# Kernel tuning notes

Hardware: AMD Instinct MI355X
Metric: run time of the kernel (lower is better)

Reference implementation:

```python
import jax, jax.numpy as jnp
import numpy as np

# Quantization constants (mirror the torch module's __init__ kwargs)
INPUT_SCALE = 0.0625          # q_in: Quantize(input_scale, 0, qint8)
SCORE_SCALE = 0.00390625      # npu_matmul output_scale for scores (1/256)
PROB_SCALE = 0.00048828125    # q_probs: Quantize(prob_scale, 0, qint8) (1/2048)
I8_MIN, I8_MAX = -128, 127
I16_MIN, I16_MAX = -32768, 32767

D, K, M, N = 256, 256, 256, 65536  # w1:[K,D], x:[D,N], w2:[M,K]


def quantize_i8(x, scale):
    # torch Quantize: round-half-to-even(x/scale) + zp(=0), clamp to int8
    return jnp.clip(jnp.round(x / scale), I8_MIN, I8_MAX).astype(jnp.int8)


def npu_matmul_i16(w_i8, x_i8):
    acc = jnp.matmul(w_i8.astype(jnp.int32), x_i8.astype(jnp.int32))
    return jnp.clip(acc, I16_MIN, I16_MAX).astype(jnp.int16)


def setup_inputs() -> dict:
    key = jax.random.key(0)
    k1, k2, k3 = jax.random.split(key, 3)
    x = jax.random.normal(k1, (D, N), dtype=jnp.float32)
    # weights are pre-quantized int8 values stored as float32 (as in the torch module)
    w1 = jax.random.randint(k2, (K, D), -16, 16).astype(jnp.float32)
    w2 = jax.random.randint(k3, (M, K), -16, 16).astype(jnp.float32)
    return {"x": x, "w1": w1, "w2": w2}


def reference(x, w1, w2):
    x_q = quantize_i8(x, INPUT_SCALE)                       # [D, N] int8
    scores_q = npu_matmul_i16(w1.astype(jnp.int8), x_q)     # [K, N] int16 (quantized, scale=SCORE_SCALE)
    scores = scores_q.astype(jnp.float32) * SCORE_SCALE     # dequantize
    probs = jax.nn.softmax(scores, axis=0)                  # softmax over dim 0
    q_probs = quantize_i8(probs, PROB_SCALE)                # [K, N] int8
    out = npu_matmul_i16(w2.astype(jnp.int8), q_probs)      # [M, N] int16
    return out
```

## Files before the change

### kernel.cpp

```cpp
#include <hip/hip_runtime.h>

typedef int   int4v   __attribute__((ext_vector_type(4)));
typedef float float4v __attribute__((ext_vector_type(4)));

#define N_DIM 65536

__device__ __forceinline__ int quant8(float v) {
    int q = (int)rintf(v);
    q = q > 127 ? 127 : q;
    q = q < -128 ? -128 : q;
    return q;
}

__device__ __forceinline__ int clamp16(int s) {
    s = s > 32767 ? 32767 : s;
    s = s < -32768 ? -32768 : s;
    return s;
}

__device__ __forceinline__ unsigned int qpack(float4v v) {
    int q0 = quant8(v.x * 16.0f);
    int q1 = quant8(v.y * 16.0f);
    int q2 = quant8(v.z * 16.0f);
    int q3 = quant8(v.w * 16.0f);
    return (unsigned int)((q0 & 0xff) | ((q1 & 0xff) << 8) |
                          ((q2 & 0xff) << 16) | ((q3 & 0xff) << 24));
}

__device__ __forceinline__ float fexp2(float a) {
    float r;
    asm("v_exp_f32 %0, %1" : "=v"(r) : "v"(a));
    return r;
}

__global__ __launch_bounds__(256) void quant_weights(const float* __restrict__ w1,
                                                     const float* __restrict__ w2,
                                                     unsigned char* __restrict__ w1q,
                                                     unsigned char* __restrict__ w2q) {
    int idx = blockIdx.x * 256 + threadIdx.x;
    const float* src;
    unsigned char* dst;
    int off;
    if (idx < 16384) { src = w1; dst = w1q; off = idx * 4; }
    else             { src = w2; dst = w2q; off = (idx - 16384) * 4; }
    float4v f = *reinterpret_cast<const float4v*>(src + off);
    unsigned int dw = (unsigned int)(((int)f.x & 0xff) | (((int)f.y & 0xff) << 8) |
                                     (((int)f.z & 0xff) << 16) | (((int)f.w & 0xff) << 24));
    *reinterpret_cast<unsigned int*>(dst + off) = dw;
}

__global__ __launch_bounds__(512, 3) void qdq_main(const float* __restrict__ x,
                                                   const unsigned char* __restrict__ w1q,
                                                   const unsigned char* __restrict__ w2q,
                                                   int* __restrict__ out) {
    __shared__ unsigned char xq[8192];
    __shared__ unsigned char pq[8192];
    __shared__ int   mb[8][32];
    __shared__ float sb[8][32];

    const int tid  = threadIdx.x;
    const int wv   = tid >> 6;
    const int lane = tid & 63;
    const int c    = lane & 15;
    const int g    = lane >> 4;

    const int rsub = lane >> 3;
    const int cg   = lane & 7;
    const int R    = rsub & 3;
    const unsigned int sel1 = (R & 1) ? 0x03070206u : 0x05010400u;
    const unsigned int sel2 = (R & 2) ? 0x07060302u : 0x01000504u;
    const int colsel = (0x3120 >> (R * 4)) & 0xF;
    const int n_t = cg * 4 + colsel;
    const int qb  = rsub & 4;

    int4v a1f[2][4];
    {
        const unsigned char* a1 = w1q + (size_t)(wv * 32 + c) * 256 + g * 16;
        #pragma unroll
        for (int rt = 0; rt < 2; ++rt)
            #pragma unroll
            for (int kk = 0; kk < 4; ++kk)
                a1f[rt][kk] = *reinterpret_cast<const int4v*>(a1 + rt * 4096 + kk * 64);
    }
    const unsigned char* a2 = w2q + (size_t)(wv * 32 + c) * 256 + g * 16;

    const int colstart = blockIdx.x * 128;
    const float* xpb = x + (size_t)(wv * 32 + rsub) * N_DIM + cg * 4;

    float4v raw[4];
    #pragma unroll
    for (int i = 0; i < 4; ++i)
        raw[i] = *reinterpret_cast<const float4v*>(xpb + (size_t)i * (8 * N_DIM) + colstart);

    const float C = 0.0056355275034725134f;

    for (int it = 0; it < 4; ++it) {
        const int col0 = colstart + it * 32;

        unsigned int Wq[4];
        #pragma unroll
        for (int i = 0; i < 4; ++i) Wq[i] = qpack(raw[i]);
        if (it < 3) {
            #pragma unroll
            for (int i = 0; i < 4; ++i)
                raw[i] = *reinterpret_cast<const float4v*>(
                    xpb + (size_t)i * (8 * N_DIM) + (col0 + 32));
        }

        #pragma unroll
        for (int i = 0; i < 4; ++i) {
            unsigned int t = (unsigned int)__shfl_xor((int)Wq[i], 8);
            unsigned int Q = __builtin_amdgcn_perm(t, Wq[i], sel1);
            unsigned int u = (unsigned int)__shfl_xor((int)Q, 16);
            unsigned int F = __builtin_amdgcn_perm(Q, u, sel2);
            const int dbase = wv * 32 + i * 8 + qb;
            *reinterpret_cast<unsigned int*>(
                xq + n_t * 256 + (dbase ^ ((n_t & 15) << 4))) = F;
        }
        __syncthreads();

        int4v bq[2][4];
        #pragma unroll
        for (int t2 = 0; t2 < 2; ++t2)
            #pragma unroll
            for (int kk = 0; kk < 4; ++kk)
                bq[t2][kk] = *reinterpret_cast<const int4v*>(
                    xq + (t2 * 16 + c) * 256 + ((kk * 64 + g * 16) ^ (c << 4)));

        unsigned int scA[4], scB[4];
        int imA = -(1 << 30), imB = -(1 << 30);
        #pragma unroll
        for (int rt = 0; rt < 2; ++rt) {
            int4v accA = {0, 0, 0, 0}, accB = {0, 0, 0, 0};
            #pragma unroll
            for (int kk = 0; kk < 4; ++kk) {
                accA = __builtin_amdgcn_mfma_i32_16x16x64_i8(a1f[rt][kk], bq[0][kk], accA, 0, 0, 0);
                accB = __builtin_amdgcn_mfma_i32_16x16x64_i8(a1f[rt][kk], bq[1][kk], accB, 0, 0, 0);
            }
            {
                const int s0 = clamp16(accA[0]), s1 = clamp16(accA[1]);
                const int s2 = clamp16(accA[2]), s3 = clamp16(accA[3]);
                int m01 = s0 > s1 ? s0 : s1, m23 = s2 > s3 ? s2 : s3;
                int m = m01 > m23 ? m01 : m23;
                imA = imA > m ? imA : m;
                scA[2 * rt]     = (unsigned int)((s0 & 0xffff) | (s1 << 16));
                scA[2 * rt + 1] = (unsigned int)((s2 & 0xffff) | (s3 << 16));
            }
            {
                const int s0 = clamp16(accB[0]), s1 = clamp16(accB[1]);
                const int s2 = clamp16(accB[2]), s3 = clamp16(accB[3]);
                int m01 = s0 > s1 ? s0 : s1, m23 = s2 > s3 ? s2 : s3;
                int m = m01 > m23 ? m01 : m23;
                imB = imB > m ? imB : m;
                scB[2 * rt]     = (unsigned int)((s0 & 0xffff) | (s1 << 16));
                scB[2 * rt + 1] = (unsigned int)((s2 & 0xffff) | (s3 << 16));
            }
        }

        {
            int o = __shfl_xor(imA, 16); imA = imA > o ? imA : o;
            o = __shfl_xor(imA, 32);     imA = imA > o ? imA : o;
            o = __shfl_xor(imB, 16);     imB = imB > o ? imB : o;
            o = __shfl_xor(imB, 32);     imB = imB > o ? imB : o;
        }
        if (g == 0) mb[wv][c] = imA;
        else if (g == 1) mb[wv][16 + c] = imB;
        float eA[8], eB[8];
        float sA = 0.0f, sB = 0.0f;
        #pragma unroll
        for (int i = 0; i < 4; ++i) {
            eA[2 * i]     = fexp2((float)((int)(short)(scA[i] & 0xffffu) - imA) * C);
            eA[2 * i + 1] = fexp2((float)(((int)scA[i] >> 16) - imA) * C);
            sA += eA[2 * i] + eA[2 * i + 1];
            eB[2 * i]     = fexp2((float)((int)(short)(scB[i] & 0xffffu) - imB) * C);
            eB[2 * i + 1] = fexp2((float)(((int)scB[i] >> 16) - imB) * C);
            sB += eB[2 * i] + eB[2 * i + 1];
        }
        sA += __shfl_xor(sA, 16); sA += __shfl_xor(sA, 32);
        sB += __shfl_xor(sB, 16); sB += __shfl_xor(sB, 32);
        if (g == 0) sb[wv][c] = sA;
        else if (g == 1) sb[wv][16 + c] = sB;

        int4v a2f[2][4];
        #pragma unroll
        for (int rt = 0; rt < 2; ++rt)
            #pragma unroll
            for (int kk = 0; kk < 4; ++kk)
                a2f[rt][kk] = *reinterpret_cast<const int4v*>(a2 + rt * 4096 + kk * 64);
        __syncthreads();

        int gmA = -(1 << 30), gmB = -(1 << 30);
        #pragma unroll
        for (int j = 0; j < 8; ++j) {
            int a = mb[j][c], b = mb[j][16 + c];
            gmA = gmA > a ? gmA : a;
            gmB = gmB > b ? gmB : b;
        }
        float gsA = 0.0f, gsB = 0.0f;
        #pragma unroll
        for (int j = 0; j < 8; ++j) {
            gsA += sb[j][c]      * fexp2((float)(mb[j][c] - gmA) * C);
            gsB += sb[j][16 + c] * fexp2((float)(mb[j][16 + c] - gmB) * C);
        }
        const float qsA = (2048.0f / gsA) * fexp2((float)(imA - gmA) * C);
        const float qsB = (2048.0f / gsB) * fexp2((float)(imB - gmB) * C);

        #pragma unroll
        for (int rt = 0; rt < 2; ++rt) {
            const int koff = wv * 32 + rt * 16 + g * 4;
            {
                int q0 = (int)rintf(eA[4 * rt + 0] * qsA);
                int q1 = (int)rintf(eA[4 * rt + 1] * qsA);
                int q2 = (int)rintf(eA[4 * rt + 2] * qsA);
                int q3 = (int)rintf(eA[4 * rt + 3] * qsA);
                q0 = q0 > 127 ? 127 : q0;
                q1 = q1 > 127 ? 127 : q1;
                q2 = q2 > 127 ? 127 : q2;
                q3 = q3 > 127 ? 127 : q3;
                *reinterpret_cast<unsigned int*>(
                    pq + c * 256 + (koff ^ (c << 4))) =
                    (unsigned int)(q0 | (q1 << 8) | (q2 << 16) | (q3 << 24));
            }
            {
                int q0 = (int)rintf(eB[4 * rt + 0] * qsB);
                int q1 = (int)rintf(eB[4 * rt + 1] * qsB);
                int q2 = (int)rintf(eB[4 * rt + 2] * qsB);
                int q3 = (int)rintf(eB[4 * rt + 3] * qsB);
                q0 = q0 > 127 ? 127 : q0;
                q1 = q1 > 127 ? 127 : q1;
                q2 = q2 > 127 ? 127 : q2;
                q3 = q3 > 127 ? 127 : q3;
                *reinterpret_cast<unsigned int*>(
                    pq + (16 + c) * 256 + (koff ^ (c << 4))) =
                    (unsigned int)(q0 | (q1 << 8) | (q2 << 16) | (q3 << 24));
            }
        }
        __syncthreads();

        int4v b2[2][4];
        #pragma unroll
        for (int t2 = 0; t2 < 2; ++t2)
            #pragma unroll
            for (int kk = 0; kk < 4; ++kk)
                b2[t2][kk] = *reinterpret_cast<const int4v*>(
                    pq + (t2 * 16 + c) * 256 + ((kk * 64 + g * 16) ^ (c << 4)));

        #pragma unroll
        for (int rt = 0; rt < 2; ++rt) {
            int4v accA = {0, 0, 0, 0}, accB = {0, 0, 0, 0};
            #pragma unroll
            for (int kk = 0; kk < 4; ++kk) {
                accA = __builtin_amdgcn_mfma_i32_16x16x64_i8(a2f[rt][kk], b2[0][kk], accA, 0, 0, 0);
                accB = __builtin_amdgcn_mfma_i32_16x16x64_i8(a2f[rt][kk], b2[1][kk], accB, 0, 0, 0);
            }
            #pragma unroll
            for (int r = 0; r < 4; ++r) {
                const size_t rowoff =
                    (size_t)(wv * 32 + rt * 16 + g * 4 + r) * N_DIM + col0;
                __builtin_nontemporal_store(clamp16(accA[r]), &out[rowoff + c]);
                __builtin_nontemporal_store(clamp16(accB[r]), &out[rowoff + 16 + c]);
            }
        }
    }
}

extern "C" void kernel_launch(void* const* d_in, const int* in_sizes, int n_in,
                              void* d_out, int out_size, void* d_ws, size_t ws_size,
                              hipStream_t stream) {
    const float* x  = (const float*)d_in[0];
    const float* w1 = (const float*)d_in[1];
    const float* w2 = (const float*)d_in[2];
    int* out = (int*)d_out;

    unsigned char* w1q = (unsigned char*)d_ws;
    unsigned char* w2q = w1q + 65536;

    quant_weights<<<128, 256, 0, stream>>>(w1, w2, w1q, w2q);
    qdq_main<<<512, 512, 0, stream>>>(x, w1q, w2q, out);
}
```

Before: 46.73 us.

## Use magic-number float quantization, recompute exps, raise occupancy, drop nontemporal stores

Replaces the rintf-and-clamp int8 quantization with an FMA against a magic constant, float min/max clamping and byte permutes for packing. It recomputes the exp values for the probabilities instead of holding 16 floats in registers, which frees registers so launch bounds can request 4 blocks per SM instead of 3. Output stores become ordinary stores instead of nontemporal ones. The trade-off is extra exp work and a change in how output writes are cached.

```diff
diff --git a/kernel.cpp b/kernel.cpp
--- a/kernel.cpp
+++ b/kernel.cpp
@@ -5,12 +5,9 @@
 
 #define N_DIM 65536
 
-__device__ __forceinline__ int quant8(float v) {
-    int q = (int)rintf(v);
-    q = q > 127 ? 127 : q;
-    q = q < -128 ? -128 : q;
-    return q;
-}
+#define QMAGIC 12582912.0f
+#define QHI    12583039.0f
+#define QLO    12582784.0f
 
 __device__ __forceinline__ int clamp16(int s) {
     s = s > 32767 ? 32767 : s;
@@ -18,13 +15,30 @@
     return s;
 }
 
+__device__ __forceinline__ unsigned int pack_low_bytes(float f0, float f1,
+                                                       float f2, float f3) {
+    unsigned int p01 = __builtin_amdgcn_perm(__float_as_uint(f1),
+                                             __float_as_uint(f0), 0x00000400u);
+    unsigned int p23 = __builtin_amdgcn_perm(__float_as_uint(f3),
+                                             __float_as_uint(f2), 0x00000400u);
+    return __builtin_amdgcn_perm(p23, p01, 0x05040100u);
+}
+
 __device__ __forceinline__ unsigned int qpack(float4v v) {
-    int q0 = quant8(v.x * 16.0f);
-    int q1 = quant8(v.y * 16.0f);
-    int q2 = quant8(v.z * 16.0f);
-    int q3 = quant8(v.w * 16.0f);
-    return (unsigned int)((q0 & 0xff) | ((q1 & 0xff) << 8) |
-                          ((q2 & 0xff) << 16) | ((q3 & 0xff) << 24));
+    float f0 = fminf(fmaxf(fmaf(v.x, 16.0f, QMAGIC), QLO), QHI);
+    float f1 = fminf(fmaxf(fmaf(v.y, 16.0f, QMAGIC), QLO), QHI);
+    float f2 = fminf(fmaxf(fmaf(v.z, 16.0f, QMAGIC), QLO), QHI);
+    float f3 = fminf(fmaxf(fmaf(v.w, 16.0f, QMAGIC), QLO), QHI);
+    return pack_low_bytes(f0, f1, f2, f3);
+}
+
+__device__ __forceinline__ unsigned int qpack_probs(float e0, float e1,
+                                                    float e2, float e3, float qs) {
+    float f0 = fminf(fmaf(e0, qs, QMAGIC), QHI);
+    float f1 = fminf(fmaf(e1, qs, QMAGIC), QHI);
+    float f2 = fminf(fmaf(e2, qs, QMAGIC), QHI);
+    float f3 = fminf(fmaf(e3, qs, QMAGIC), QHI);
+    return pack_low_bytes(f0, f1, f2, f3);
 }
 
 __device__ __forceinline__ float fexp2(float a) {
@@ -49,7 +63,7 @@
     *reinterpret_cast<unsigned int*>(dst + off) = dw;
 }
 
-__global__ __launch_bounds__(512, 3) void qdq_main(const float* __restrict__ x,
+__global__ __launch_bounds__(512, 4) void qdq_main(const float* __restrict__ x,
                                                    const unsigned char* __restrict__ w1q,
                                                    const unsigned char* __restrict__ w2q,
                                                    int* __restrict__ out) {
@@ -165,16 +179,13 @@
         }
         if (g == 0) mb[wv][c] = imA;
         else if (g == 1) mb[wv][16 + c] = imB;
-        float eA[8], eB[8];
         float sA = 0.0f, sB = 0.0f;
         #pragma unroll
         for (int i = 0; i < 4; ++i) {
-            eA[2 * i]     = fexp2((float)((int)(short)(scA[i] & 0xffffu) - imA) * C);
-            eA[2 * i + 1] = fexp2((float)(((int)scA[i] >> 16) - imA) * C);
-            sA += eA[2 * i] + eA[2 * i + 1];
-            eB[2 * i]     = fexp2((float)((int)(short)(scB[i] & 0xffffu) - imB) * C);
-            eB[2 * i + 1] = fexp2((float)(((int)scB[i] >> 16) - imB) * C);
-            sB += eB[2 * i] + eB[2 * i + 1];
+            sA += fexp2((float)((int)(short)(scA[i] & 0xffffu) - imA) * C);
+            sA += fexp2((float)(((int)scA[i] >> 16) - imA) * C);
+            sB += fexp2((float)((int)(short)(scB[i] & 0xffffu) - imB) * C);
+            sB += fexp2((float)(((int)scB[i] >> 16) - imB) * C);
         }
         sA += __shfl_xor(sA, 16); sA += __shfl_xor(sA, 32);
         sB += __shfl_xor(sB, 16); sB += __shfl_xor(sB, 32);
@@ -209,30 +220,20 @@
         for (int rt = 0; rt < 2; ++rt) {
             const int koff = wv * 32 + rt * 16 + g * 4;
             {
-                int q0 = (int)rintf(eA[4 * rt + 0] * qsA);
-                int q1 = (int)rintf(eA[4 * rt + 1] * qsA);
-                int q2 = (int)rintf(eA[4 * rt + 2] * qsA);
-                int q3 = (int)rintf(eA[4 * rt + 3] * qsA);
-                q0 = q0 > 127 ? 127 : q0;
-                q1 = q1 > 127 ? 127 : q1;
-                q2 = q2 > 127 ? 127 : q2;
-                q3 = q3 > 127 ? 127 : q3;
+                float e0 = fexp2((float)((int)(short)(scA[2 * rt] & 0xffffu) - imA) * C);
+                float e1 = fexp2((float)(((int)scA[2 * rt] >> 16) - imA) * C);
+                float e2 = fexp2((float)((int)(short)(scA[2 * rt + 1] & 0xffffu) - imA) * C);
+                float e3 = fexp2((float)(((int)scA[2 * rt + 1] >> 16) - imA) * C);
                 *reinterpret_cast<unsigned int*>(
-                    pq + c * 256 + (koff ^ (c << 4))) =
-                    (unsigned int)(q0 | (q1 << 8) | (q2 << 16) | (q3 << 24));
-            }
-            {
-                int q0 = (int)rintf(eB[4 * rt + 0] * qsB);
-                int q1 = (int)rintf(eB[4 * rt + 1] * qsB);
-                int q2 = (int)rintf(eB[4 * rt + 2] * qsB);
-                int q3 = (int)rintf(eB[4 * rt + 3] * qsB);
-                q0 = q0 > 127 ? 127 : q0;
-                q1 = q1 > 127 ? 127 : q1;
-                q2 = q2 > 127 ? 127 : q2;
-                q3 = q3 > 127 ? 127 : q3;
+                    pq + c * 256 + (koff ^ (c << 4))) = qpack_probs(e0, e1, e2, e3, qsA);
+            }
+            {
+                float e0 = fexp2((float)((int)(short)(scB[2 * rt] & 0xffffu) - imB) * C);
+                float e1 = fexp2((float)(((int)scB[2 * rt] >> 16) - imB) * C);
+                float e2 = fexp2((float)((int)(short)(scB[2 * rt + 1] & 0xffffu) - imB) * C);
+                float e3 = fexp2((float)(((int)scB[2 * rt + 1] >> 16) - imB) * C);
                 *reinterpret_cast<unsigned int*>(
-                    pq + (16 + c) * 256 + (koff ^ (c << 4))) =
-                    (unsigned int)(q0 | (q1 << 8) | (q2 << 16) | (q3 << 24));
+                    pq + (16 + c) * 256 + (koff ^ (c << 4))) = qpack_probs(e0, e1, e2, e3, qsB);
             }
         }
         __syncthreads();
@@ -257,8 +258,8 @@
             for (int r = 0; r < 4; ++r) {
                 const size_t rowoff =
                     (size_t)(wv * 32 + rt * 16 + g * 4 + r) * N_DIM + col0;
-                __builtin_nontemporal_store(clamp16(accA[r]), &out[rowoff + c]);
-                __builtin_nontemporal_store(clamp16(accB[r]), &out[rowoff + 16 + c]);
+                out[rowoff + c]      = clamp16(accA[r]);
+                out[rowoff + 16 + c] = clamp16(accB[r]);
             }
         }
     }
```

Result: slower. 81.23 us (+73.8%).
